# Performance work log

Hardware: AMD Instinct MI355X
Metric: run time of the kernel (lower is better)

Reference implementation:

```python
import jax, jax.numpy as jnp
import numpy as np

N_NODES = 50000
N_EDGES = 800000
NFEAT = 256
NHID = 512
BN_EPS = 1e-5


def setup_inputs() -> dict:
    key = jax.random.key(0)
    ks = jax.random.split(key, 6)
    x = jax.random.normal(ks[0], (N_NODES, NFEAT), dtype=jnp.float32)
    edge_index = jax.random.randint(ks[1], (2, N_EDGES), 0, N_NODES, dtype=jnp.int64)
    # Xavier-uniform linear weights, zero biases (matches weights_init)
    lim1 = np.sqrt(6.0 / (NFEAT + NHID))
    W1 = jax.random.uniform(ks[2], (NFEAT, NHID), minval=-lim1, maxval=lim1, dtype=jnp.float32)
    b1 = jnp.zeros((NHID,), dtype=jnp.float32)
    lim2 = np.sqrt(6.0 / (NHID + NHID))
    W2 = jax.random.uniform(ks[3], (NHID, NHID), minval=-lim2, maxval=lim2, dtype=jnp.float32)
    b2 = jnp.zeros((NHID,), dtype=jnp.float32)
    gamma = jnp.ones((NHID,), dtype=jnp.float32)
    beta = jnp.zeros((NHID,), dtype=jnp.float32)
    return {"x": x, "edge_index": edge_index, "W1": W1, "b1": b1,
            "gamma": gamma, "beta": beta, "W2": W2, "b2": b2}


def reference(x, edge_index, W1, b1, gamma, beta, W2, b2):
    # GINConv (eps=0): h_i = MLP(x_i + sum_{j->i} x_j)
    src = edge_index[0]
    dst = edge_index[1]
    agg = jax.ops.segment_sum(x[src], dst, num_segments=x.shape[0])  # [N, nfeat]
    h = x + agg
    # MLP: Linear -> ReLU -> BatchNorm1d (training-mode batch stats) -> Linear
    h = jax.nn.relu(h @ W1 + b1)  # [N, nhid]
    mean = jnp.mean(h, axis=0)
    var = jnp.var(h, axis=0)  # biased, as PyTorch uses for normalization
    h = (h - mean) * jax.lax.rsqrt(var + BN_EPS) * gamma + beta
    return h @ W2 + b2
```

## Files before the change

kernel.cpp:

```cpp
#include <hip/hip_runtime.h>

#define NNODES 50000
#define NF 256
#define NH 512
#define MPAD 50048
#define NRB 391
#define BN_EPS 1e-5f
#define CAP 96

typedef unsigned short u16;
typedef __attribute__((ext_vector_type(8))) short bf16x8;
typedef __attribute__((ext_vector_type(4))) float f32x4;

__device__ __forceinline__ float bf2f(u16 u) {
  union { unsigned int i; float f; } v; v.i = ((unsigned int)u) << 16; return v.f;
}
__device__ __forceinline__ u16 f2bf(float f) {
  union { float ff; unsigned int i; } v; v.ff = f;
  unsigned int r = v.i + 0x7FFFu + ((v.i >> 16) & 1u);
  return (u16)(r >> 16);
}

__device__ __forceinline__ void async16(const void* g, void* l) {
  __builtin_amdgcn_global_load_lds(
      (const __attribute__((address_space(1))) unsigned int*)g,
      (__attribute__((address_space(3))) unsigned int*)l, 16, 0, 0);
}

__global__ __launch_bounds__(256) void conv_tr_kernel(const float* __restrict__ x,
                                                      u16* __restrict__ xbf,
                                                      const float* __restrict__ W1,
                                                      u16* __restrict__ W1t) {
  const int b = blockIdx.x;
  if (b < 2048) {
    const size_t n8 = (size_t)NNODES * NF / 8;
    size_t stride = (size_t)2048 * 256;
    for (size_t i = b * (size_t)256 + threadIdx.x; i < n8; i += stride) {
      float4 a = ((const float4*)x)[2 * i];
      float4 c = ((const float4*)x)[2 * i + 1];
      ushort4 lo, hi;
      lo.x = f2bf(a.x); lo.y = f2bf(a.y); lo.z = f2bf(a.z); lo.w = f2bf(a.w);
      hi.x = f2bf(c.x); hi.y = f2bf(c.y); hi.z = f2bf(c.z); hi.w = f2bf(c.w);
      ((ushort4*)xbf)[2 * i] = lo;
      ((ushort4*)xbf)[2 * i + 1] = hi;
    }
  } else {
    int idx = (b - 2048) * 256 + threadIdx.x;
    int n = idx >> 8;
    int k = idx & 255;
    W1t[(size_t)n * NF + k] = f2bf(W1[(size_t)k * NH + n]);
  }
}

__global__ __launch_bounds__(256) void bucket_fill(const int* __restrict__ ei, int E,
                                                   int* __restrict__ cw,
                                                   int* __restrict__ srcs,
                                                   int* __restrict__ err) {
  __shared__ int sf;
  if (threadIdx.x < 64) {
    unsigned long long bb = __ballot(ei[2 * threadIdx.x + 1] == 0);
    if (threadIdx.x == 0) sf = (bb == ~0ull) ? 1 : 0;
  }
  __syncthreads();
  const int is64 = sf;
  const int gtid = blockIdx.x * 256 + threadIdx.x;
  const int stride = gridDim.x * 256;
  if (is64) {
    const int4* s4 = (const int4*)ei;
    const int4* d4 = (const int4*)(ei + 2 * (size_t)E);
    int np = E >> 1;
    for (int p = gtid; p < np; p += stride) {
      int4 sv = s4[p], dv = d4[p];
      if ((unsigned)sv.x < NNODES && (unsigned)dv.x < NNODES) {
        int pos = atomicAdd(&cw[dv.x], 1);
        if (pos < CAP) srcs[(size_t)dv.x * CAP + pos] = sv.x; else err[0] = 4;
      }
      if ((unsigned)sv.z < NNODES && (unsigned)dv.z < NNODES) {
        int pos = atomicAdd(&cw[dv.z], 1);
        if (pos < CAP) srcs[(size_t)dv.z * CAP + pos] = sv.z; else err[0] = 4;
      }
    }
    for (int e = (np << 1) + gtid; e < E; e += stride) {
      int src = ei[2 * e], dst = ei[2 * (size_t)E + 2 * e];
      if ((unsigned)src >= NNODES || (unsigned)dst >= NNODES) continue;
      int pos = atomicAdd(&cw[dst], 1);
      if (pos < CAP) srcs[(size_t)dst * CAP + pos] = src; else err[0] = 4;
    }
  } else {
    const int4* s4 = (const int4*)ei;
    const int4* d4 = (const int4*)(ei + E);
    int np = E >> 2;
    for (int p = gtid; p < np; p += stride) {
      int4 sv = s4[p], dv = d4[p];
      int ss[4] = {sv.x, sv.y, sv.z, sv.w};
      int dd[4] = {dv.x, dv.y, dv.z, dv.w};
#pragma unroll
      for (int j = 0; j < 4; ++j) {
        if ((unsigned)ss[j] < NNODES && (unsigned)dd[j] < NNODES) {
          int pos = atomicAdd(&cw[dd[j]], 1);
          if (pos < CAP) srcs[(size_t)dd[j] * CAP + pos] = ss[j]; else err[0] = 4;
        }
      }
    }
    for (int e = (np << 2) + gtid; e < E; e += stride) {
      int src = ei[e], dst = ei[(size_t)E + e];
      if ((unsigned)src >= NNODES || (unsigned)dst >= NNODES) continue;
      int pos = atomicAdd(&cw[dst], 1);
      if (pos < CAP) srcs[(size_t)dst * CAP + pos] = src; else err[0] = 4;
    }
  }
}

__global__ __launch_bounds__(256) void gather_kernel(const u16* __restrict__ xbf,
                                                     const int* __restrict__ srcs,
                                                     const int* __restrict__ cw,
                                                     u16* __restrict__ hpad) {
  const int hl = threadIdx.x & 31;
  const int node = blockIdx.x * 8 + (threadIdx.x >> 5);
  if (node >= MPAD) return;
  bf16x8* outp = (bf16x8*)(hpad + (size_t)node * NF + hl * 8);
  if (node >= NNODES) {
    bf16x8 z = {0, 0, 0, 0, 0, 0, 0, 0};
    *outp = z;
    return;
  }
  bf16x8 sv = *(const bf16x8*)(xbf + (size_t)node * NF + hl * 8);
  float acc[8];
#pragma unroll
  for (int j = 0; j < 8; ++j) acc[j] = bf2f((u16)sv[j]);
  int cnt = cw[node];
  if (cnt > CAP) cnt = CAP;
  const int* lst = srcs + (size_t)node * CAP;
  int e = 0;
  for (; e + 3 < cnt; e += 4) {
    bf16x8 v[4];
#pragma unroll
    for (int u = 0; u < 4; ++u)
      v[u] = *(const bf16x8*)(xbf + (size_t)lst[e + u] * NF + hl * 8);
#pragma unroll
    for (int u = 0; u < 4; ++u)
#pragma unroll
      for (int j = 0; j < 8; ++j) acc[j] += bf2f((u16)v[u][j]);
  }
  for (; e < cnt; ++e) {
    bf16x8 v0 = *(const bf16x8*)(xbf + (size_t)lst[e] * NF + hl * 8);
#pragma unroll
    for (int j = 0; j < 8; ++j) acc[j] += bf2f((u16)v0[j]);
  }
  bf16x8 o;
#pragma unroll
  for (int j = 0; j < 8; ++j) o[j] = (short)f2bf(acc[j]);
  *outp = o;
}

template <int K, bool RELU, bool OUTF32, bool STATS>
__global__ __launch_bounds__(256) void gemm_bt(const u16* __restrict__ Ab,
                                               const u16* __restrict__ Bt,
                                               const float* __restrict__ bias,
                                               void* __restrict__ Cp, int Mstore,
                                               float* __restrict__ parts) {
  __shared__ __align__(16) u16 As[128 * 64];
  __shared__ __align__(16) u16 Bs[128 * 64];
  __shared__ float sred[256];
  const int tid = threadIdx.x;
  const int lane = tid & 63;
  const int wid = tid >> 6;
  const int wr = wid >> 1, wc = wid & 1;

  const int nwg = gridDim.x;
  const int q = nwg >> 3, r = nwg & 7;
  const int xcd = blockIdx.x & 7, idx = blockIdx.x >> 3;
  const int work = (xcd < r ? xcd * (q + 1) : r * (q + 1) + (xcd - r) * q) + idx;
  const int brow = (work >> 2) * 128;
  const int bcol = (work & 3) * 128;

  f32x4 acc[4][4] = {};

  const int lrow = lane >> 3;
  const int lkc = ((lane & 7) ^ (lrow & 7)) * 8;
  const int nt = K / 64;

  if (STATS) {
    if (tid < 64) ((float4*)sred)[tid] = (float4){0.f, 0.f, 0.f, 0.f};
  }

  for (int t = 0; t < nt; ++t) {
    const int k0 = t * 64;
#pragma unroll
    for (int i = 0; i < 4; ++i) {
      int c = i * 4 + wid;
      int row = c * 8 + lrow;
      async16(Ab + (size_t)(brow + row) * K + k0 + lkc, &As[c * 512]);
      async16(Bt + (size_t)(bcol + row) * K + k0 + lkc, &Bs[c * 512]);
    }
    __syncthreads();
#pragma unroll
    for (int ks = 0; ks < 2; ++ks) {
      bf16x8 af[4], bfr[4];
      const int rchunk = ((ks << 2) + (lane >> 4)) ^ (lane & 7);
#pragma unroll
      for (int m = 0; m < 4; ++m)
        af[m] = *(const bf16x8*)&As[(wr * 64 + m * 16 + (lane & 15)) * 64 + rchunk * 8];
#pragma unroll
      for (int n = 0; n < 4; ++n)
        bfr[n] = *(const bf16x8*)&Bs[(wc * 64 + n * 16 + (lane & 15)) * 64 + rchunk * 8];
#pragma unroll
      for (int n = 0; n < 4; ++n)
#pragma unroll
        for (int m = 0; m < 4; ++m)
          acc[n][m] = __builtin_amdgcn_mfma_f32_16x16x32_bf16(bfr[n], af[m], acc[n][m], 0, 0, 0);
    }
    __syncthreads();
  }

  const int row_base = brow + wr * 64 + (lane & 15);
  const int col_base = bcol + wc * 64 + ((lane >> 4) << 2);
#pragma unroll
  for (int n = 0; n < 4; ++n) {
    int col = col_base + n * 16;
    float4 bv4 = *(const float4*)&bias[col];
    float s0 = 0.f, s1 = 0.f, s2 = 0.f, s3 = 0.f;
    float q0 = 0.f, q1 = 0.f, q2 = 0.f, q3 = 0.f;
#pragma unroll
    for (int m = 0; m < 4; ++m) {
      int row = row_base + m * 16;
      f32x4 a = acc[n][m];
      float v0 = a[0] + bv4.x, v1 = a[1] + bv4.y, v2 = a[2] + bv4.z, v3 = a[3] + bv4.w;
      if (RELU) {
        v0 = fmaxf(v0, 0.f); v1 = fmaxf(v1, 0.f);
        v2 = fmaxf(v2, 0.f); v3 = fmaxf(v3, 0.f);
      }
      if (row < Mstore) {
        if (OUTF32) {
          float4 o = {v0, v1, v2, v3};
          *(float4*)&((float*)Cp)[(size_t)row * NH + col] = o;
        } else {
          ushort4 o = {f2bf(v0), f2bf(v1), f2bf(v2), f2bf(v3)};
          *(ushort4*)&((u16*)Cp)[(size_t)row * NH + col] = o;
        }
      }
      if (STATS && row < NNODES) {
        s0 += v0; s1 += v1; s2 += v2; s3 += v3;
        q0 += v0 * v0; q1 += v1 * v1; q2 += v2 * v2; q3 += v3 * v3;
      }
    }
    if (STATS) {
#pragma unroll
      for (int msk = 1; msk < 16; msk <<= 1) {
        s0 += __shfl_xor(s0, msk); s1 += __shfl_xor(s1, msk);
        s2 += __shfl_xor(s2, msk); s3 += __shfl_xor(s3, msk);
        q0 += __shfl_xor(q0, msk); q1 += __shfl_xor(q1, msk);
        q2 += __shfl_xor(q2, msk); q3 += __shfl_xor(q3, msk);
      }
      if ((lane & 15) == 0) {
        int lc = wc * 64 + n * 16 + ((lane >> 4) << 2);
        atomicAdd(&sred[lc + 0], s0); atomicAdd(&sred[lc + 1], s1);
        atomicAdd(&sred[lc + 2], s2); atomicAdd(&sred[lc + 3], s3);
        atomicAdd(&sred[128 + lc + 0], q0); atomicAdd(&sred[128 + lc + 1], q1);
        atomicAdd(&sred[128 + lc + 2], q2); atomicAdd(&sred[128 + lc + 3], q3);
      }
    }
  }
  if (STATS) {
    __syncthreads();
    if (tid < 128) {
      parts[(size_t)work * 256 + tid] = sred[tid];
      parts[(size_t)work * 256 + 128 + tid] = sred[128 + tid];
    }
  }
}

__global__ __launch_bounds__(256) void stats_bn(const float* __restrict__ parts,
                                                const float* __restrict__ gamma,
                                                const float* __restrict__ beta,
                                                float* __restrict__ a_arr,
                                                float* __restrict__ c_arr,
                                                int* __restrict__ err) {
  int c = blockIdx.x * 256 + threadIdx.x;
  int grp = (c >> 7) & 3, cl = c & 127;
  float s = 0.f, qq = 0.f;
  for (int rb = 0; rb < NRB; ++rb) {
    const float* p = parts + (size_t)((rb << 2) + grp) * 256 + cl;
    s += p[0];
    qq += p[128];
  }
  float mean = s * (1.f / NNODES);
  float var = qq * (1.f / NNODES) - mean * mean;
  if (!(mean == mean) || !(var == var) ||
      fabsf(mean) > 1e20f || var > 1e20f || var < -1e-2f)
    err[0] = 2;
  if (var < 0.f) var = 0.f;
  float a = gamma[c] * rsqrtf(var + BN_EPS);
  a_arr[c] = a;
  c_arr[c] = beta[c] - mean * a;
}

__global__ __launch_bounds__(256) void fold_w2(const float* __restrict__ W2,
                                               const float* __restrict__ b2,
                                               const float* __restrict__ a_arr,
                                               const float* __restrict__ c_arr,
                                               u16* __restrict__ W2pt,
                                               float* __restrict__ bias2p) {
  int n = blockIdx.x;
  int t = threadIdx.x;
  float accv = 0.f;
  for (int k = t; k < NH; k += 256) {
    float w = W2[(size_t)k * NH + n];
    W2pt[(size_t)n * NH + k] = f2bf(a_arr[k] * w);
    accv += c_arr[k] * w;
  }
  __shared__ float red[256];
  red[t] = accv;
  __syncthreads();
  for (int s = 128; s > 0; s >>= 1) {
    if (t < s) red[t] += red[t + s];
    __syncthreads();
  }
  if (t == 0) bias2p[n] = b2[n] + red[0];
}

__global__ __launch_bounds__(256) void write_sentinel(float* __restrict__ out, int n, float val) {
  int stride = gridDim.x * blockDim.x;
  for (int i = blockIdx.x * blockDim.x + threadIdx.x; i < n; i += stride) out[i] = val;
}

__global__ __launch_bounds__(256) void apply_err(const int* __restrict__ err,
                                                 float* __restrict__ out, int n) {
  if (err[0] == 0) return;
  int stride = gridDim.x * blockDim.x;
  for (int i = blockIdx.x * blockDim.x + threadIdx.x; i < n; i += stride) out[i] = -500000.f;
}

extern "C" void kernel_launch(void* const* d_in, const int* in_sizes, int n_in,
                              void* d_out, int out_size, void* d_ws, size_t ws_size,
                              hipStream_t stream) {
  const float* x     = (const float*)d_in[0];
  const int*   ei    = (const int*)d_in[1];
  const float* W1    = (const float*)d_in[2];
  const float* b1    = (const float*)d_in[3];
  const float* gamma = (const float*)d_in[4];
  const float* beta  = (const float*)d_in[5];
  const float* W2    = (const float*)d_in[6];
  const float* b2    = (const float*)d_in[7];
  float* out = (float*)d_out;
  const int E = in_sizes[1] / 2;

  char* ws = (char*)d_ws;
  size_t off = 0;
  auto alloc = [&](size_t bytes) {
    char* p = ws + off;
    off += (bytes + 255) & ~(size_t)255;
    return p;
  };
  u16*   xbf    = (u16*)alloc((size_t)NNODES * NF * 2);
  u16*   hpad   = (u16*)alloc((size_t)MPAD * NF * 2);
  u16*   h1     = (u16*)alloc((size_t)MPAD * NH * 2);
  u16*   W1t    = (u16*)alloc((size_t)NH * NF * 2);
  u16*   W2pt   = (u16*)alloc((size_t)NH * NH * 2);
  int*   srcs   = (int*)alloc((size_t)NNODES * CAP * 4);
  int*   cw     = (int*)alloc((size_t)NNODES * 4);
  float* parts  = (float*)alloc((size_t)NRB * 4 * 256 * 4);
  int*   err    = (int*)alloc(8);
  float* a_arr  = (float*)alloc(NH * 4);
  float* c_arr  = (float*)alloc(NH * 4);
  float* bias2p = (float*)alloc(NH * 4);

  if (off > ws_size) {
    write_sentinel<<<2048, 256, 0, stream>>>(out, out_size,
        1.0e7f + 1048576.0f * (float)(ws_size >> 20));
    return;
  }

  hipMemsetAsync(cw, 0, (size_t)NNODES * 4, stream);
  hipMemsetAsync(err, 0, 8, stream);

  bucket_fill<<<1024, 256, 0, stream>>>(ei, E, cw, srcs, err);
  conv_tr_kernel<<<2560, 256, 0, stream>>>(x, xbf, W1, W1t);
  gather_kernel<<<MPAD / 8, 256, 0, stream>>>(xbf, srcs, cw, hpad);

  const int nwg = NRB * 4;
  gemm_bt<NF, true, false, true><<<nwg, 256, 0, stream>>>(hpad, W1t, b1, h1, MPAD, parts);

  stats_bn<<<2, 256, 0, stream>>>(parts, gamma, beta, a_arr, c_arr, err);
  fold_w2<<<NH, 256, 0, stream>>>(W2, b2, a_arr, c_arr, W2pt, bias2p);

  gemm_bt<NH, false, true, false><<<nwg, 256, 0, stream>>>(h1, W2pt, bias2p, out, NNODES, nullptr);

  apply_err<<<2048, 256, 0, stream>>>(err, out, out_size);
}
```

Measured before the change: 234.6 us.

## Double-buffer LDS tiles in GEMM to overlap global loads with MFMA

```diff
diff --git a/kernel.cpp b/kernel.cpp
--- a/kernel.cpp
+++ b/kernel.cpp
@@ -159,8 +159,8 @@
                                                const float* __restrict__ bias,
                                                void* __restrict__ Cp, int Mstore,
                                                float* __restrict__ parts) {
-  __shared__ __align__(16) u16 As[128 * 64];
-  __shared__ __align__(16) u16 Bs[128 * 64];
+  __shared__ __align__(16) u16 As[2][128 * 64];
+  __shared__ __align__(16) u16 Bs[2][128 * 64];
   __shared__ float sred[256];
   const int tid = threadIdx.x;
   const int lane = tid & 63;
@@ -184,33 +184,54 @@
     if (tid < 64) ((float4*)sred)[tid] = (float4){0.f, 0.f, 0.f, 0.f};
   }
 
+#pragma unroll
+  for (int i = 0; i < 4; ++i) {
+    int c = i * 4 + wid;
+    int row = c * 8 + lrow;
+    async16(Ab + (size_t)(brow + row) * K + lkc, &As[0][c * 512]);
+    async16(Bt + (size_t)(bcol + row) * K + lkc, &Bs[0][c * 512]);
+  }
+
+  int cur = 0;
   for (int t = 0; t < nt; ++t) {
-    const int k0 = t * 64;
-#pragma unroll
-    for (int i = 0; i < 4; ++i) {
-      int c = i * 4 + wid;
-      int row = c * 8 + lrow;
-      async16(Ab + (size_t)(brow + row) * K + k0 + lkc, &As[c * 512]);
-      async16(Bt + (size_t)(bcol + row) * K + k0 + lkc, &Bs[c * 512]);
-    }
-    __syncthreads();
+    if (t + 1 < nt) {
+      const int k0 = (t + 1) * 64;
+#pragma unroll
+      for (int i = 0; i < 4; ++i) {
+        int c = i * 4 + wid;
+        int row = c * 8 + lrow;
+        async16(Ab + (size_t)(brow + row) * K + k0 + lkc, &As[cur ^ 1][c * 512]);
+        async16(Bt + (size_t)(bcol + row) * K + k0 + lkc, &Bs[cur ^ 1][c * 512]);
+      }
+      asm volatile("s_waitcnt vmcnt(8)" ::: "memory");
+    } else {
+      asm volatile("s_waitcnt vmcnt(0)" ::: "memory");
+    }
+    __builtin_amdgcn_sched_barrier(0);
+    __builtin_amdgcn_s_barrier();
+    __builtin_amdgcn_sched_barrier(0);
+
 #pragma unroll
     for (int ks = 0; ks < 2; ++ks) {
       bf16x8 af[4], bfr[4];
       const int rchunk = ((ks << 2) + (lane >> 4)) ^ (lane & 7);
 #pragma unroll
       for (int m = 0; m < 4; ++m)
-        af[m] = *(const bf16x8*)&As[(wr * 64 + m * 16 + (lane & 15)) * 64 + rchunk * 8];
+        af[m] = *(const bf16x8*)&As[cur][(wr * 64 + m * 16 + (lane & 15)) * 64 + rchunk * 8];
 #pragma unroll
       for (int n = 0; n < 4; ++n)
-        bfr[n] = *(const bf16x8*)&Bs[(wc * 64 + n * 16 + (lane & 15)) * 64 + rchunk * 8];
+        bfr[n] = *(const bf16x8*)&Bs[cur][(wc * 64 + n * 16 + (lane & 15)) * 64 + rchunk * 8];
 #pragma unroll
       for (int n = 0; n < 4; ++n)
 #pragma unroll
         for (int m = 0; m < 4; ++m)
           acc[n][m] = __builtin_amdgcn_mfma_f32_16x16x32_bf16(bfr[n], af[m], acc[n][m], 0, 0, 0);
     }
-    __syncthreads();
+    asm volatile("s_waitcnt lgkmcnt(0)" ::: "memory");
+    __builtin_amdgcn_sched_barrier(0);
+    __builtin_amdgcn_s_barrier();
+    __builtin_amdgcn_sched_barrier(0);
+    cur ^= 1;
   }
 
   const int row_base = brow + wr * 64 + (lane & 15);
```

Measured after the change: 237.6 us. No clear change (+1.3%).
